# Optimization experiments

Measured on AMD Instinct MI355X. Metric: run time of the kernel, lower is better.

Reference implementation:

```python
import jax, jax.numpy as jnp
import numpy as np

N_NODES = 50000


def _inv_sqrt_deg(idx, n):
    # degree per node from an edge-endpoint index vector; 0-degree -> norm 0 (DGL behavior)
    deg = jax.ops.segment_sum(jnp.ones(idx.shape[0], jnp.float32), idx, num_segments=n)
    return jnp.where(deg > 0, jax.lax.rsqrt(jnp.maximum(deg, 1.0)), 0.0)


def _graph_conv(x, src, dst, W, b, norm_src, norm_dst, n):
    # DGL GraphConv, norm='both': D_dst^{-1/2} A D_src^{-1/2} X W + b
    h = (x * norm_src[:, None]) @ W            # [N, out]
    agg = jax.ops.segment_sum(h[src], dst, num_segments=n)  # SpMM via gather+scatter-add
    return agg * norm_dst[:, None] + b


def setup_inputs() -> dict:
    key = jax.random.key(0)
    ks = jax.random.split(key, 8)
    N, E, D, H, C = N_NODES, 800000, 64, 64, 10
    s = 1.0 / np.sqrt(H)
    return {
        "x": jax.random.normal(ks[0], (N, D), jnp.float32),
        "src": jax.random.randint(ks[1], (E,), 0, N, jnp.int32),
        "dst": jax.random.randint(ks[2], (E,), 0, N, jnp.int32),
        "W1": jax.random.normal(ks[3], (D, H), jnp.float32) * s,
        "b1": jnp.zeros((H,), jnp.float32),
        "W2": jax.random.normal(ks[4], (H, H), jnp.float32) * s,
        "b2": jnp.zeros((H,), jnp.float32),
        "W3": jax.random.normal(ks[5], (H, H), jnp.float32) * s,
        "b3": jnp.zeros((H,), jnp.float32),
        "Wfc": jax.random.normal(ks[6], (H, C), jnp.float32) * s,
        "bfc": jnp.zeros((C,), jnp.float32),
    }


def reference(x, src, dst, W1, b1, W2, b2, W3, b3, Wfc, bfc):
    n = x.shape[0]
    norm_src = _inv_sqrt_deg(src, n)  # out-degree^{-1/2}
    norm_dst = _inv_sqrt_deg(dst, n)  # in-degree^{-1/2}
    h = jnp.tanh(_graph_conv(x, src, dst, W1, b1, norm_src, norm_dst, n))
    h = jnp.tanh(_graph_conv(h, src, dst, W2, b2, norm_src, norm_dst, n))
    h = jnp.tanh(_graph_conv(h, src, dst, W3, b3, norm_src, norm_dst, n))
    return h @ Wfc + bfc
```

## Files before the change

kernel.cpp:

```cpp
#include <hip/hip_runtime.h>
#include <hip/hip_fp16.h>
#include <math.h>

#define THREADS 256
#define CHUNK_SHIFT 15
#define CHUNK (1 << CHUNK_SHIFT)
#define LDS_WORDS 12500
#define MAXB 16
#define XS_STRIDE 68

__global__ __launch_bounds__(1024)
void k_hist(const int* __restrict__ src, const int* __restrict__ dst,
            unsigned int* __restrict__ partS, unsigned int* __restrict__ partD,
            unsigned char* __restrict__ rank, unsigned int* __restrict__ counter,
            int E, int P, int words) {
    __shared__ unsigned int hist[LDS_WORDS];
    if (blockIdx.x == 0 && threadIdx.x == 0) *counter = 0u;
    int isSrc = (blockIdx.x >= (unsigned)P);
    int b = isSrc ? (blockIdx.x - P) : blockIdx.x;
    int tid = threadIdx.x;

    for (int w = tid; w < words; w += 1024) hist[w] = 0u;
    __syncthreads();

    int start = b << CHUNK_SHIFT;
    int end = start + CHUNK; if (end > E) end = E;

    if (isSrc) {
        for (int e = start + tid; e < end; e += 1024) {
            int s = src[e];
            atomicAdd(&hist[s >> 2], 1u << ((s & 3) * 8));
        }
    } else {
        for (int e = start + tid; e < end; e += 1024) {
            int d = dst[e];
            unsigned int old = atomicAdd(&hist[d >> 2], 1u << ((d & 3) * 8));
            rank[e] = (unsigned char)((old >> ((d & 3) * 8)) & 0xFFu);
        }
    }
    __syncthreads();

    unsigned int* part = isSrc ? partS : partD;
    for (int w = tid; w < words; w += 1024)
        part[(size_t)b * words + w] = hist[w];
}

__global__ __launch_bounds__(THREADS)
void k_pre(const unsigned int* __restrict__ partS,
           const unsigned int* __restrict__ partD,
           unsigned int* __restrict__ prefD,
           int* __restrict__ deg_d, float* __restrict__ ns, float* __restrict__ nd,
           int* __restrict__ rp, int* __restrict__ bsum,
           unsigned int* __restrict__ counter,
           int P, int words, int N) {
    __shared__ unsigned int qsD[4][64];
    __shared__ unsigned int qsS[4][64];
    int t = threadIdx.x;
    int widx = t & 63;
    int q = t >> 6;
    int w = blockIdx.x * 64 + widx;
    bool valid = (w < words);

    int per = (P + 3) >> 2;
    int blo = q * per;
    int cnt = P - blo; if (cnt > per) cnt = per; if (cnt < 0) cnt = 0;

    unsigned int vD[MAXB];
    unsigned int runD = 0, runS = 0;
#pragma unroll
    for (int bb = 0; bb < MAXB; bb++) {
        unsigned int vd = 0, vs = 0;
        if (bb < cnt && valid) {
            size_t off = (size_t)(blo + bb) * words + w;
            vd = partD[off];
            vs = partS[off];
        }
        vD[bb] = vd;
        runD += vd;
        runS += vs;
    }
    qsD[q][widx] = runD;
    qsS[q][widx] = runS;
    __syncthreads();

    unsigned int baseD = 0, totD = 0, totS = 0;
#pragma unroll
    for (int qq = 0; qq < 4; qq++) {
        unsigned int xd = qsD[qq][widx];
        unsigned int xs = qsS[qq][widx];
        if (qq < q) baseD += xd;
        totD += xd;
        totS += xs;
    }

    unsigned int pref = baseD;
#pragma unroll
    for (int bb = 0; bb < MAXB; bb++) {
        if (bb < cnt && valid)
            prefD[(size_t)(blo + bb) * words + w] = pref;
        pref += vD[bb];
    }

    if (q == 0) {
        int b0 = (int)(totD & 0xFFu), b1 = (int)((totD >> 8) & 0xFFu),
            b2 = (int)((totD >> 16) & 0xFFu), b3 = (int)((totD >> 24) & 0xFFu);
        int wsum = b0 + b1 + b2 + b3;
        int incl = wsum;
#pragma unroll
        for (int off = 1; off < 64; off <<= 1) {
            int y = __shfl_up(incl, off);
            if (widx >= off) incl += y;
        }
        int excl = incl - wsum;
        int btot = __shfl(incl, 63);
        if (widx == 0)
            bsum[blockIdx.x] = (int)atomicAdd(counter, (unsigned int)btot);
        if (valid) {
            int s0 = (int)(totS & 0xFFu), s1 = (int)((totS >> 8) & 0xFFu),
                s2 = (int)((totS >> 16) & 0xFFu), s3 = (int)((totS >> 24) & 0xFFu);
            int4 dv; dv.x = b0; dv.y = b1; dv.z = b2; dv.w = b3;
            *(int4*)&deg_d[(size_t)4 * w] = dv;
            float4 ndv;
            ndv.x = b0 ? 1.0f / sqrtf((float)b0) : 0.0f;
            ndv.y = b1 ? 1.0f / sqrtf((float)b1) : 0.0f;
            ndv.z = b2 ? 1.0f / sqrtf((float)b2) : 0.0f;
            ndv.w = b3 ? 1.0f / sqrtf((float)b3) : 0.0f;
            *(float4*)&nd[(size_t)4 * w] = ndv;
            float4 nsv;
            nsv.x = s0 ? 1.0f / sqrtf((float)s0) : 0.0f;
            nsv.y = s1 ? 1.0f / sqrtf((float)s1) : 0.0f;
            nsv.z = s2 ? 1.0f / sqrtf((float)s2) : 0.0f;
            nsv.w = s3 ? 1.0f / sqrtf((float)s3) : 0.0f;
            *(float4*)&ns[(size_t)4 * w] = nsv;
            int4 rv; rv.x = excl; rv.y = excl + b0;
            rv.z = excl + b0 + b1; rv.w = excl + b0 + b1 + b2;
            *(int4*)&rp[(size_t)4 * w] = rv;
        }
    }
}

__global__ __launch_bounds__(256, 4)
void k_fill_gemm(const int* __restrict__ src, const int* __restrict__ dst,
                 const int* __restrict__ rp, const int* __restrict__ bsum,
                 const unsigned char* __restrict__ rank,
                 const unsigned int* __restrict__ prefD,
                 int* __restrict__ col, int E, int words, int gFill,
                 const float* __restrict__ X, const float* __restrict__ norm,
                 const float* __restrict__ W, __half* __restrict__ H, int N) {
    __shared__ float Xs[64 * XS_STRIDE];
    __shared__ float Ws[64 * 64];
    int tid = threadIdx.x;

    if ((int)blockIdx.x < gFill) {
        int e = blockIdx.x * 256 + tid;
        if (e < E) {
            int d = dst[e];
            int b = e >> CHUNK_SHIFT;
            unsigned int pk = prefD[(size_t)b * words + (d >> 2)];
            int pref = (int)((pk >> ((d & 3) * 8)) & 0xFFu);
            col[rp[d] + bsum[d >> 8] + pref + (int)rank[e]] = src[e];
        }
        return;
    }

    int rowBase = ((int)blockIdx.x - gFill) * 64;
    for (int i = tid; i < 1024; i += 256)
        ((float4*)Ws)[i] = ((const float4*)W)[i];
    for (int i = tid; i < 1024; i += 256) {
        int r = i >> 4, k4 = i & 15;
        int row = rowBase + r;
        float4 v = make_float4(0.f, 0.f, 0.f, 0.f);
        if (row < N) {
            v = ((const float4*)X)[(size_t)row * 16 + k4];
            float nv = norm[row];
            v.x *= nv; v.y *= nv; v.z *= nv; v.w *= nv;
        }
        *((float4*)&Xs[r * XS_STRIDE + (k4 << 2)]) = v;
    }
    __syncthreads();

    int tc = tid & 15, tr = tid >> 4;
    int c0 = tc * 4, r0 = tr * 4;
    float acc[4][4] = {};

#pragma unroll 2
    for (int k = 0; k < 64; k += 4) {
        float4 wv[4];
#pragma unroll
        for (int kk = 0; kk < 4; kk++)
            wv[kk] = *((const float4*)&Ws[(k + kk) * 64 + c0]);
#pragma unroll
        for (int j = 0; j < 4; j++) {
            float4 xv = *((const float4*)&Xs[(r0 + j) * XS_STRIDE + k]);
            acc[j][0] += xv.x * wv[0].x; acc[j][1] += xv.x * wv[0].y;
            acc[j][2] += xv.x * wv[0].z; acc[j][3] += xv.x * wv[0].w;
            acc[j][0] += xv.y * wv[1].x; acc[j][1] += xv.y * wv[1].y;
            acc[j][2] += xv.y * wv[1].z; acc[j][3] += xv.y * wv[1].w;
            acc[j][0] += xv.z * wv[2].x; acc[j][1] += xv.z * wv[2].y;
            acc[j][2] += xv.z * wv[2].z; acc[j][3] += xv.z * wv[2].w;
            acc[j][0] += xv.w * wv[3].x; acc[j][1] += xv.w * wv[3].y;
            acc[j][2] += xv.w * wv[3].z; acc[j][3] += xv.w * wv[3].w;
        }
    }
#pragma unroll
    for (int j = 0; j < 4; j++) {
        int row = rowBase + r0 + j;
        if (row < N) {
            __half2 h01 = __floats2half2_rn(acc[j][0], acc[j][1]);
            __half2 h23 = __floats2half2_rn(acc[j][2], acc[j][3]);
            uint2 pk;
            pk.x = *(unsigned int*)&h01;
            pk.y = *(unsigned int*)&h23;
            *((uint2*)(H + (size_t)row * 64 + c0)) = pk;
        }
    }
}

template<int FC>
__global__ __launch_bounds__(256, 6)
void k_agg_gemm(const uint4* __restrict__ H4, const int* __restrict__ rp,
                const int* __restrict__ bsum, const int* __restrict__ deg,
                const int* __restrict__ col, const float* __restrict__ nd,
                const float* __restrict__ nsrc, const float* __restrict__ bias,
                const float* __restrict__ W, const float* __restrict__ Wb2,
                void* __restrict__ OutP, int N) {
    __shared__ float Xs[32 * XS_STRIDE];
    __shared__ float Ws[FC ? 680 : 4096];
    __shared__ float Wb[16];
    int tid = threadIdx.x;

    if constexpr (FC == 0) {
        for (int i = tid; i < 1024; i += 256)
            ((float4*)Ws)[i] = ((const float4*)W)[i];
    } else {
        for (int i = tid; i < 640; i += 256) {
            int k = i / 10, c = i - k * 10;
            Ws[c * 68 + k] = W[i];
        }
        if (tid < 10) Wb[tid] = Wb2[tid];
    }

    int wave = tid >> 6;
    int lane = tid & 63;
    int g = lane >> 3;
    int l = lane & 7;
    int rowBase = blockIdx.x * 32;

    float4 bv0 = *((const float4*)&bias[l * 8]);
    float4 bv1 = *((const float4*)&bias[l * 8 + 4]);

    int node = rowBase + wave * 8 + g;
    int st = 0, n = 0; float nv = 0.f, nsv = 0.f;
    if (node < N) {
        st  = rp[node] + bsum[node >> 8];
        n   = deg[node];
        nv  = nd[node];
        if constexpr (FC == 0) nsv = nsrc[node];
    }
    int idx = (l < n) ? col[st + l] : 0;

    int m = n;
#pragma unroll
    for (int d = 8; d <= 32; d <<= 1) {
        int tm = __shfl_xor(m, d); m = m > tm ? m : tm;
    }

    {
        float acc[8] = {0.f, 0.f, 0.f, 0.f, 0.f, 0.f, 0.f, 0.f};
        for (int j0 = 0; j0 < m; j0 += 8) {
            int idxn = ((j0 + 8 + l) < n) ? col[st + j0 + 8 + l] : 0;
#pragma unroll
            for (int jj = 0; jj < 8; jj++) {
                int s = __shfl(idx, (g << 3) + jj);
                if (j0 + jj < n) {
                    uint4 v = H4[(size_t)s * 8 + l];
                    float2 f0 = __half22float2(*(__half2*)&v.x);
                    float2 f1 = __half22float2(*(__half2*)&v.y);
                    float2 f2 = __half22float2(*(__half2*)&v.z);
                    float2 f3 = __half22float2(*(__half2*)&v.w);
                    acc[0] += f0.x; acc[1] += f0.y; acc[2] += f1.x; acc[3] += f1.y;
                    acc[4] += f2.x; acc[5] += f2.y; acc[6] += f3.x; acc[7] += f3.y;
                }
            }
            idx = idxn;
        }
        float4 o0, o1;
        o0.x = tanhf(acc[0] * nv + bv0.x);
        o0.y = tanhf(acc[1] * nv + bv0.y);
        o0.z = tanhf(acc[2] * nv + bv0.z);
        o0.w = tanhf(acc[3] * nv + bv0.w);
        o1.x = tanhf(acc[4] * nv + bv1.x);
        o1.y = tanhf(acc[5] * nv + bv1.y);
        o1.z = tanhf(acc[6] * nv + bv1.z);
        o1.w = tanhf(acc[7] * nv + bv1.w);
        if constexpr (FC == 0) {
            o0.x *= nsv; o0.y *= nsv; o0.z *= nsv; o0.w *= nsv;
            o1.x *= nsv; o1.y *= nsv; o1.z *= nsv; o1.w *= nsv;
        }
        if (node >= N) {
            o0 = make_float4(0.f, 0.f, 0.f, 0.f);
            o1 = make_float4(0.f, 0.f, 0.f, 0.f);
        }
        int row = wave * 8 + g;
        *((float4*)&Xs[row * XS_STRIDE + l * 8])     = o0;
        *((float4*)&Xs[row * XS_STRIDE + l * 8 + 4]) = o1;
    }
    __syncthreads();

    if constexpr (FC == 0) {
        __half* Hh = (__half*)OutP;
        int tc = tid & 15, tr = tid >> 4;
        int c0 = tc * 4, r0 = tr * 2;
        float acc[2][4] = {};

#pragma unroll 2
        for (int k = 0; k < 64; k += 4) {
            float4 wv[4];
#pragma unroll
            for (int kk = 0; kk < 4; kk++)
                wv[kk] = *((const float4*)&Ws[(k + kk) * 64 + c0]);
#pragma unroll
            for (int j = 0; j < 2; j++) {
                float4 xv = *((const float4*)&Xs[(r0 + j) * XS_STRIDE + k]);
                acc[j][0] += xv.x * wv[0].x; acc[j][1] += xv.x * wv[0].y;
                acc[j][2] += xv.x * wv[0].z; acc[j][3] += xv.x * wv[0].w;
                acc[j][0] += xv.y * wv[1].x; acc[j][1] += xv.y * wv[1].y;
                acc[j][2] += xv.y * wv[1].z; acc[j][3] += xv.y * wv[1].w;
                acc[j][0] += xv.z * wv[2].x; acc[j][1] += xv.z * wv[2].y;
                acc[j][2] += xv.z * wv[2].z; acc[j][3] += xv.z * wv[2].w;
                acc[j][0] += xv.w * wv[3].x; acc[j][1] += xv.w * wv[3].y;
                acc[j][2] += xv.w * wv[3].z; acc[j][3] += xv.w * wv[3].w;
            }
        }
#pragma unroll
        for (int j = 0; j < 2; j++) {
            int row = rowBase + r0 + j;
            if (row < N) {
                __half2 h01 = __floats2half2_rn(acc[j][0], acc[j][1]);
                __half2 h23 = __floats2half2_rn(acc[j][2], acc[j][3]);
                uint2 pk;
                pk.x = *(unsigned int*)&h01;
                pk.y = *(unsigned int*)&h23;
                *((uint2*)(Hh + (size_t)row * 64 + c0)) = pk;
            }
        }
    } else {
        float* outF = (float*)OutP;
        for (int idx2 = tid; idx2 < 320; idx2 += 256) {
            int ln = idx2 / 10;
            int cl = idx2 - ln * 10;
            float acc = Wb[cl];
#pragma unroll
            for (int k = 0; k < 64; k += 4) {
                float4 xv = *((const float4*)&Xs[ln * XS_STRIDE + k]);
                float4 wv = *((const float4*)&Ws[cl * 68 + k]);
                acc += xv.x * wv.x + xv.y * wv.y + xv.z * wv.z + xv.w * wv.w;
            }
            int row = rowBase + ln;
            if (row < N) outF[(size_t)row * 10 + cl] = acc;
        }
    }
}

extern "C" void kernel_launch(void* const* d_in, const int* in_sizes, int n_in,
                              void* d_out, int out_size, void* d_ws, size_t ws_size,
                              hipStream_t stream) {
    const float* x   = (const float*)d_in[0];
    const int*   src = (const int*)d_in[1];
    const int*   dst = (const int*)d_in[2];
    const float* W1  = (const float*)d_in[3];
    const float* b1  = (const float*)d_in[4];
    const float* W2  = (const float*)d_in[5];
    const float* b2  = (const float*)d_in[6];
    const float* W3  = (const float*)d_in[7];
    const float* b3  = (const float*)d_in[8];
    const float* Wfc = (const float*)d_in[9];
    const float* bfc = (const float*)d_in[10];
    float* out = (float*)d_out;
    int N = in_sizes[0] / 64;
    int E = in_sizes[1];
    int P = (E + CHUNK - 1) >> CHUNK_SHIFT;
    int words = (N + 3) / 4;

    char* ws = (char*)d_ws;
    size_t p = 0;
    auto alloc = [&](size_t bytes) -> void* {
        void* r = ws + p;
        p = (p + bytes + 255) & ~(size_t)255;
        return r;
    };
    int*    deg_d = (int*)alloc((size_t)N * 4);
    int*    rp    = (int*)alloc((size_t)N * 4);
    int*    bsum  = (int*)alloc((size_t)THREADS * 4);
    unsigned char* rank = (unsigned char*)alloc((size_t)E);
    int*    col   = (int*)alloc((size_t)E * 4);
    float*  ns    = (float*)alloc((size_t)N * 4);
    float*  nd    = (float*)alloc((size_t)N * 4);
    unsigned int* partS = (unsigned int*)alloc((size_t)P * words * 4);
    unsigned int* partD = (unsigned int*)alloc((size_t)P * words * 4);
    unsigned int* prefD = (unsigned int*)alloc((size_t)P * words * 4);
    __half* bufH  = (__half*)alloc((size_t)N * 64 * 2);
    __half* bufH2 = (__half*)alloc((size_t)N * 64 * 2);
    unsigned int* counter = (unsigned int*)alloc(4);
    (void)ws_size; (void)n_in; (void)out_size;

    int gFill = (E + 255) / 256;
    int gP = (words + 63) / 64;
    int gGemm = (N + 63) / 64;
    int gAgg  = (N + 31) / 32;

    k_hist<<<2 * P, 1024, 0, stream>>>(src, dst, partS, partD, rank, counter, E, P, words);
    k_pre <<<gP, THREADS, 0, stream>>>(partS, partD, prefD, deg_d, ns, nd,
                                       rp, bsum, counter, P, words, N);
    k_fill_gemm<<<gFill + gGemm, 256, 0, stream>>>(src, dst, rp, bsum, rank, prefD,
                                                   col, E, words, gFill,
                                                   x, ns, W1, bufH, N);
    k_agg_gemm<0><<<gAgg, 256, 0, stream>>>((const uint4*)bufH,  rp, bsum, deg_d, col,
                                            nd, ns, b1, W2, nullptr, bufH2, N);
    k_agg_gemm<0><<<gAgg, 256, 0, stream>>>((const uint4*)bufH2, rp, bsum, deg_d, col,
                                            nd, ns, b2, W3, nullptr, bufH, N);
    k_agg_gemm<1><<<gAgg, 256, 0, stream>>>((const uint4*)bufH,  rp, bsum, deg_d, col,
                                            nd, ns, b3, Wfc, bfc, out, N);
}
```

Measured before the change: 199.9 us.

## Make aggregate-GEMM wave-local to drop mid-kernel barrier, use 512-thread blocks

Result: faster. 187.6 us (-6.2%).

```diff
diff --git a/kernel.cpp b/kernel.cpp
--- a/kernel.cpp
+++ b/kernel.cpp
@@ -217,39 +217,41 @@
 }
 
 template<int FC>
-__global__ __launch_bounds__(256, 6)
+__global__ __launch_bounds__(512)
 void k_agg_gemm(const uint4* __restrict__ H4, const int* __restrict__ rp,
                 const int* __restrict__ bsum, const int* __restrict__ deg,
                 const int* __restrict__ col, const float* __restrict__ nd,
                 const float* __restrict__ nsrc, const float* __restrict__ bias,
                 const float* __restrict__ W, const float* __restrict__ Wb2,
                 void* __restrict__ OutP, int N) {
-    __shared__ float Xs[32 * XS_STRIDE];
+    __shared__ float Xs[64 * XS_STRIDE];
     __shared__ float Ws[FC ? 680 : 4096];
     __shared__ float Wb[16];
     int tid = threadIdx.x;
 
     if constexpr (FC == 0) {
-        for (int i = tid; i < 1024; i += 256)
+        for (int i = tid; i < 1024; i += 512)
             ((float4*)Ws)[i] = ((const float4*)W)[i];
     } else {
-        for (int i = tid; i < 640; i += 256) {
+        for (int i = tid; i < 640; i += 512) {
             int k = i / 10, c = i - k * 10;
             Ws[c * 68 + k] = W[i];
         }
         if (tid < 10) Wb[tid] = Wb2[tid];
     }
+    __syncthreads();
 
     int wave = tid >> 6;
     int lane = tid & 63;
     int g = lane >> 3;
     int l = lane & 7;
-    int rowBase = blockIdx.x * 32;
+    int rowBase = blockIdx.x * 64;
+    int row = wave * 8 + g;
 
     float4 bv0 = *((const float4*)&bias[l * 8]);
     float4 bv1 = *((const float4*)&bias[l * 8 + 4]);
 
-    int node = rowBase + wave * 8 + g;
+    int node = rowBase + row;
     int st = 0, n = 0; float nv = 0.f, nsv = 0.f;
     if (node < N) {
         st  = rp[node] + bsum[node >> 8];
@@ -301,63 +303,55 @@
             o0 = make_float4(0.f, 0.f, 0.f, 0.f);
             o1 = make_float4(0.f, 0.f, 0.f, 0.f);
         }
-        int row = wave * 8 + g;
         *((float4*)&Xs[row * XS_STRIDE + l * 8])     = o0;
         *((float4*)&Xs[row * XS_STRIDE + l * 8 + 4]) = o1;
     }
-    __syncthreads();
 
     if constexpr (FC == 0) {
         __half* Hh = (__half*)OutP;
-        int tc = tid & 15, tr = tid >> 4;
-        int c0 = tc * 4, r0 = tr * 2;
-        float acc[2][4] = {};
-
+        float a2[8] = {0.f, 0.f, 0.f, 0.f, 0.f, 0.f, 0.f, 0.f};
 #pragma unroll 2
         for (int k = 0; k < 64; k += 4) {
-            float4 wv[4];
-#pragma unroll
-            for (int kk = 0; kk < 4; kk++)
-                wv[kk] = *((const float4*)&Ws[(k + kk) * 64 + c0]);
-#pragma unroll
-            for (int j = 0; j < 2; j++) {
-                float4 xv = *((const float4*)&Xs[(r0 + j) * XS_STRIDE + k]);
-                acc[j][0] += xv.x * wv[0].x; acc[j][1] += xv.x * wv[0].y;
-                acc[j][2] += xv.x * wv[0].z; acc[j][3] += xv.x * wv[0].w;
-                acc[j][0] += xv.y * wv[1].x; acc[j][1] += xv.y * wv[1].y;
-                acc[j][2] += xv.y * wv[1].z; acc[j][3] += xv.y * wv[1].w;
-                acc[j][0] += xv.z * wv[2].x; acc[j][1] += xv.z * wv[2].y;
-                acc[j][2] += xv.z * wv[2].z; acc[j][3] += xv.z * wv[2].w;
-                acc[j][0] += xv.w * wv[3].x; acc[j][1] += xv.w * wv[3].y;
-                acc[j][2] += xv.w * wv[3].z; acc[j][3] += xv.w * wv[3].w;
+            float4 xv = *((const float4*)&Xs[row * XS_STRIDE + k]);
+#pragma unroll
+            for (int kk = 0; kk < 4; kk++) {
+                float4 w0 = *((const float4*)&Ws[(k + kk) * 64 + l * 8]);
+                float4 w1 = *((const float4*)&Ws[(k + kk) * 64 + l * 8 + 4]);
+                float xk = (kk == 0) ? xv.x : (kk == 1) ? xv.y : (kk == 2) ? xv.z : xv.w;
+                a2[0] += xk * w0.x; a2[1] += xk * w0.y;
+                a2[2] += xk * w0.z; a2[3] += xk * w0.w;
+                a2[4] += xk * w1.x; a2[5] += xk * w1.y;
+                a2[6] += xk * w1.z; a2[7] += xk * w1.w;
             }
         }
-#pragma unroll
-        for (int j = 0; j < 2; j++) {
-            int row = rowBase + r0 + j;
-            if (row < N) {
-                __half2 h01 = __floats2half2_rn(acc[j][0], acc[j][1]);
-                __half2 h23 = __floats2half2_rn(acc[j][2], acc[j][3]);
-                uint2 pk;
-                pk.x = *(unsigned int*)&h01;
-                pk.y = *(unsigned int*)&h23;
-                *((uint2*)(Hh + (size_t)row * 64 + c0)) = pk;
-            }
+        int grow = rowBase + row;
+        if (grow < N) {
+            __half2 h0 = __floats2half2_rn(a2[0], a2[1]);
+            __half2 h1 = __floats2half2_rn(a2[2], a2[3]);
+            __half2 h2 = __floats2half2_rn(a2[4], a2[5]);
+            __half2 h3 = __floats2half2_rn(a2[6], a2[7]);
+            uint4 pk;
+            pk.x = *(unsigned int*)&h0;
+            pk.y = *(unsigned int*)&h1;
+            pk.z = *(unsigned int*)&h2;
+            pk.w = *(unsigned int*)&h3;
+            *((uint4*)(Hh + (size_t)grow * 64 + l * 8)) = pk;
         }
     } else {
         float* outF = (float*)OutP;
-        for (int idx2 = tid; idx2 < 320; idx2 += 256) {
-            int ln = idx2 / 10;
-            int cl = idx2 - ln * 10;
+        for (int t2 = lane; t2 < 80; t2 += 64) {
+            int ln = t2 / 10;
+            int cl = t2 - ln * 10;
+            int lrow = wave * 8 + ln;
             float acc = Wb[cl];
 #pragma unroll
             for (int k = 0; k < 64; k += 4) {
-                float4 xv = *((const float4*)&Xs[ln * XS_STRIDE + k]);
+                float4 xv = *((const float4*)&Xs[lrow * XS_STRIDE + k]);
                 float4 wv = *((const float4*)&Ws[cl * 68 + k]);
                 acc += xv.x * wv.x + xv.y * wv.y + xv.z * wv.z + xv.w * wv.w;
             }
-            int row = rowBase + ln;
-            if (row < N) outF[(size_t)row * 10 + cl] = acc;
+            int grow = rowBase + lrow;
+            if (grow < N) outF[(size_t)grow * 10 + cl] = acc;
         }
     }
 }
@@ -407,7 +401,7 @@
     int gFill = (E + 255) / 256;
     int gP = (words + 63) / 64;
     int gGemm = (N + 63) / 64;
-    int gAgg  = (N + 31) / 32;
+    int gAgg  = (N + 63) / 64;
 
     k_hist<<<2 * P, 1024, 0, stream>>>(src, dst, partS, partD, rank, counter, E, P, words);
     k_pre <<<gP, THREADS, 0, stream>>>(partS, partD, prefD, deg_d, ns, nd,
@@ -415,10 +409,10 @@
     k_fill_gemm<<<gFill + gGemm, 256, 0, stream>>>(src, dst, rp, bsum, rank, prefD,
                                                    col, E, words, gFill,
                                                    x, ns, W1, bufH, N);
-    k_agg_gemm<0><<<gAgg, 256, 0, stream>>>((const uint4*)bufH,  rp, bsum, deg_d, col,
+    k_agg_gemm<0><<<gAgg, 512, 0, stream>>>((const uint4*)bufH,  rp, bsum, deg_d, col,
                                             nd, ns, b1, W2, nullptr, bufH2, N);
-    k_agg_gemm<0><<<gAgg, 256, 0, stream>>>((const uint4*)bufH2, rp, bsum, deg_d, col,
+    k_agg_gemm<0><<<gAgg, 512, 0, stream>>>((const uint4*)bufH2, rp, bsum, deg_d, col,
                                             nd, ns, b2, W3, nullptr, bufH, N);
-    k_agg_gemm<1><<<gAgg, 256, 0, stream>>>((const uint4*)bufH,  rp, bsum, deg_d, col,
+    k_agg_gemm<1><<<gAgg, 512, 0, stream>>>((const uint4*)bufH,  rp, bsum, deg_d, col,
                                             nd, ns, b3, Wfc, bfc, out, N);
 }
```
